# Optimization experiments

Hardware: AMD Instinct MI355X
Metric: run time of the kernel (lower is better)

Reference implementation:

```python
import jax, jax.numpy as jnp
import numpy as np

GENES = 20000   # input gene nodes (depth 0)
LEVEL = 10000   # nodes per subsequent depth level
STEPS = 7       # depth propagation steps
DEG = 16        # in-degree per dst node
N = GENES + STEPS * LEVEL          # 90000 total nodes
EPS = LEVEL * DEG                  # 160000 edges per step
E = STEPS * EPS                    # 1120000 total edges
B = 256
C = 2


def setup_inputs() -> dict:
    key = jax.random.key(0)
    k0, k1, k2 = jax.random.split(key, 3)
    X = jax.random.normal(k0, (B, GENES), jnp.float32)
    gene_map = jnp.arange(GENES, dtype=jnp.int32)

    rng = np.random.default_rng(0)
    src_list, dstu_list = [], []
    for k in range(STEPS):
        lo = 0 if k == 0 else GENES + (k - 1) * LEVEL
        hi = GENES if k == 0 else lo + LEVEL
        src_list.append(rng.integers(lo, hi, size=EPS))
        dstu_list.append(np.arange(GENES + k * LEVEL, GENES + (k + 1) * LEVEL))
    src = jnp.asarray(np.stack(src_list), dtype=jnp.int32)          # [STEPS, EPS]
    dst_unique = jnp.asarray(np.stack(dstu_list), dtype=jnp.int32)  # [STEPS, LEVEL]
    dst_pos = jnp.tile(jnp.repeat(jnp.arange(LEVEL, dtype=jnp.int32), DEG)[None, :], (STEPS, 1))
    eid = jnp.arange(E, dtype=jnp.int32).reshape(STEPS, EPS)
    root_ids = dst_unique[-1]

    edge_weight = jax.random.normal(k1, (E,), jnp.float32) * 0.01
    node_bias = jnp.zeros((N,), jnp.float32)
    head_W = jax.random.normal(k2, (LEVEL, C), jnp.float32) * (1.0 / np.sqrt(LEVEL))
    head_b = jnp.zeros((C,), jnp.float32)

    return dict(X=X, edge_weight=edge_weight, node_bias=node_bias,
                head_W=head_W, head_b=head_b, gene_map=gene_map,
                src=src, dst_pos=dst_pos, dst_unique=dst_unique,
                eid=eid, root_ids=root_ids)


def reference(X, edge_weight, node_bias, head_W, head_b,
              gene_map, src, dst_pos, dst_unique, eid, root_ids):
    # dropout is identity (eval mode / p=0)
    b = X.shape[0]
    h = jnp.zeros((b, N), X.dtype).at[:, gene_map].set(X)
    for k in range(src.shape[0]):  # fixed small number of depth steps
        w = edge_weight[eid[k]]                                   # [EPS]
        msg = h[:, src[k]] * w[None, :]                           # gather + scale [B, EPS]
        agg = jnp.zeros((b, dst_unique.shape[1]), h.dtype).at[:, dst_pos[k]].add(msg)
        h_dst = jnp.tanh(agg + node_bias[dst_unique[k]][None, :])  # [B, LEVEL]
        h = h.at[:, dst_unique[k]].set(h_dst)
    roots = h[:, root_ids]                                        # [B, LEVEL]
    return roots @ head_W + head_b
```

## Files before the change

kernel.cpp:

```cpp
#include <hip/hip_runtime.h>
#include <math.h>

#define GENES 20000
#define LEVEL 10000
#define STEPS 7
#define DEG   16
#define EPSZ  (LEVEL * DEG)
#define CCOLS 32
#define NCHUNK 8
#define SBLK  157
#define DBLK  313
#define NGT   625
#define MSTRIDE 18

typedef unsigned short bf8 __attribute__((ext_vector_type(8)));

__device__ inline float bf2f(unsigned short u) {
    union { unsigned u; float f; } c; c.u = ((unsigned)u) << 16; return c.f;
}
__device__ inline unsigned short f2bf(float x) {
    union { float f; unsigned u; } c; c.f = x;
    return (unsigned short)((c.u + 0x7fffu + ((c.u >> 16) & 1u)) >> 16);
}

__global__ __launch_bounds__(256) void transpose_k(const float* __restrict__ X,
                                                   const int*   __restrict__ gene_map,
                                                   unsigned short* __restrict__ XT) {
    __shared__ float tile[32][33];
    const int chunk = blockIdx.x;
    const int l4  = threadIdx.x & 7;
    const int r8  = threadIdx.x >> 3;
    const int lo  = threadIdx.x & 31;
    const int gr8 = threadIdx.x >> 5;
    unsigned short* XTp = XT + (size_t)chunk * GENES * CCOLS;
    for (int i = 0; i < 4; ++i) {
        const int gt = blockIdx.y * 4 + i;
        if (gt >= NGT) break;
        const int g0 = gt * 32;
        if (i) __syncthreads();
        const float4 xv = *reinterpret_cast<const float4*>(
            X + (size_t)(chunk * CCOLS + r8) * GENES + g0 + l4 * 4);
        tile[r8][l4 * 4 + 0] = xv.x;
        tile[r8][l4 * 4 + 1] = xv.y;
        tile[r8][l4 * 4 + 2] = xv.z;
        tile[r8][l4 * 4 + 3] = xv.w;
        __syncthreads();
#pragma unroll
        for (int jj = 0; jj < 4; ++jj) {
            const int gr   = gr8 + jj * 8;
            const int node = gene_map[g0 + gr];
            XTp[(size_t)node * CCOLS + lo] = f2bf(tile[lo][gr]);
        }
    }
}

__global__ __launch_bounds__(256) void step_k(const unsigned short* __restrict__ hprev,
                                              unsigned short*       __restrict__ hcur,
                                              const int*   __restrict__ src_k,
                                              const float* __restrict__ w_k,
                                              const float* __restrict__ node_bias,
                                              const int*   __restrict__ dstu_k,
                                              int src_base, int prev_rows) {
    const int bid   = blockIdx.x;
    const int chunk = bid & 7;
    const int cb    = bid >> 3;
    const int tid   = threadIdx.x;

    __shared__ int   s_src[32 * MSTRIDE];
    __shared__ float s_w  [32 * MSTRIDE];

    if (tid < 128) {
        const int m4 = cb * 128 + tid;
        if (m4 < EPSZ / 4) {
            const int4 sv = reinterpret_cast<const int4*>(src_k)[m4];
            const int j = tid >> 2, i = (tid & 3) * 4;
            *reinterpret_cast<int4*>(&s_src[j * MSTRIDE + i]) = sv;
        }
    } else {
        const int t  = tid - 128;
        const int m4 = cb * 128 + t;
        if (m4 < EPSZ / 4) {
            const float4 wv = reinterpret_cast<const float4*>(w_k)[m4];
            const int j = t >> 2, i = (t & 3) * 4;
            *reinterpret_cast<float4*>(&s_w[j * MSTRIDE + i]) = wv;
        }
    }
    __syncthreads();

    const int wave = tid >> 6, lane = tid & 63;
    const int c2 = lane & 3;
    const int eh = (lane >> 2) & 1;
    const int q  = lane >> 3;
    const int j  = wave * 8 + q;
    const int dest = cb * 32 + j;
    const int c8 = c2 * 8;

    if (dest < LEVEL) {
        const unsigned short* prev = hprev + (size_t)chunk * prev_rows * CCOLS;
        unsigned short*       curp = hcur + (size_t)chunk * LEVEL * CCOLS;

        const int mb = j * MSTRIDE + eh * 8;
        const int4   sA = *reinterpret_cast<const int4*>  (&s_src[mb]);
        const int4   sB = *reinterpret_cast<const int4*>  (&s_src[mb + 4]);
        const float4 wA = *reinterpret_cast<const float4*>(&s_w  [mb]);
        const float4 wB = *reinterpret_cast<const float4*>(&s_w  [mb + 4]);

#define GL(sv) (*reinterpret_cast<const bf8*>(prev + (size_t)((sv) - src_base) * CCOLS + c8))
        const bf8 v0 = GL(sA.x);
        const bf8 v1 = GL(sA.y);
        const bf8 v2 = GL(sA.z);
        const bf8 v3 = GL(sA.w);
        const bf8 v4 = GL(sB.x);
        const bf8 v5 = GL(sB.y);
        const bf8 v6 = GL(sB.z);
        const bf8 v7 = GL(sB.w);
#undef GL

        float a0 = 0.f, a1 = 0.f, a2 = 0.f, a3 = 0.f, a4 = 0.f, a5 = 0.f, a6 = 0.f, a7 = 0.f;
#define FMA8(v, wv) { a0 = fmaf(bf2f((v)[0]), (wv), a0); a1 = fmaf(bf2f((v)[1]), (wv), a1);  \
                      a2 = fmaf(bf2f((v)[2]), (wv), a2); a3 = fmaf(bf2f((v)[3]), (wv), a3);  \
                      a4 = fmaf(bf2f((v)[4]), (wv), a4); a5 = fmaf(bf2f((v)[5]), (wv), a5);  \
                      a6 = fmaf(bf2f((v)[6]), (wv), a6); a7 = fmaf(bf2f((v)[7]), (wv), a7); }
        FMA8(v0, wA.x) FMA8(v1, wA.y) FMA8(v2, wA.z) FMA8(v3, wA.w)
        FMA8(v4, wB.x) FMA8(v5, wB.y) FMA8(v6, wB.z) FMA8(v7, wB.w)
#undef FMA8

        a0 += __shfl_xor(a0, 4); a1 += __shfl_xor(a1, 4);
        a2 += __shfl_xor(a2, 4); a3 += __shfl_xor(a3, 4);
        a4 += __shfl_xor(a4, 4); a5 += __shfl_xor(a5, 4);
        a6 += __shfl_xor(a6, 4); a7 += __shfl_xor(a7, 4);

        if (eh == 0) {
            const float bz = node_bias[dstu_k[dest]];
            bf8 o;
            o[0] = f2bf(tanhf(a0 + bz));
            o[1] = f2bf(tanhf(a1 + bz));
            o[2] = f2bf(tanhf(a2 + bz));
            o[3] = f2bf(tanhf(a3 + bz));
            o[4] = f2bf(tanhf(a4 + bz));
            o[5] = f2bf(tanhf(a5 + bz));
            o[6] = f2bf(tanhf(a6 + bz));
            o[7] = f2bf(tanhf(a7 + bz));
            *reinterpret_cast<bf8*>(curp + (size_t)dest * CCOLS + c8) = o;
        }
    }
}

__global__ __launch_bounds__(256) void step7_head_k(const unsigned short* __restrict__ hprev,
                                                    const int*   __restrict__ src_k,
                                                    const float* __restrict__ w_k,
                                                    const float* __restrict__ node_bias,
                                                    const int*   __restrict__ dstu_k,
                                                    const float* __restrict__ head_W,
                                                    float*       __restrict__ part,
                                                    int src_base) {
    const int bid   = blockIdx.x;
    const int chunk = bid & 7;
    const int cb    = bid >> 3;
    const int tid   = threadIdx.x;

    __shared__ int   s_src[64 * MSTRIDE];
    __shared__ float s_w  [64 * MSTRIDE];
    __shared__ float o_tile[64][33];
    __shared__ float s_W2[64][2];
    __shared__ float red[8][64];

    {
        const int m4 = cb * 256 + tid;
        if (m4 < EPSZ / 4) {
            const int4   sv = reinterpret_cast<const int4*>(src_k)[m4];
            const float4 wv = reinterpret_cast<const float4*>(w_k)[m4];
            const int j = tid >> 2, i = (tid & 3) * 4;
            *reinterpret_cast<int4*>  (&s_src[j * MSTRIDE + i]) = sv;
            *reinterpret_cast<float4*>(&s_w  [j * MSTRIDE + i]) = wv;
        }
    }
    if (tid < 32) {
        const int f4 = cb * 32 + tid;
        float4 wv = make_float4(0.f, 0.f, 0.f, 0.f);
        if (f4 < (LEVEL * 2) / 4) wv = reinterpret_cast<const float4*>(head_W)[f4];
        s_W2[tid * 2 + 0][0] = wv.x; s_W2[tid * 2 + 0][1] = wv.y;
        s_W2[tid * 2 + 1][0] = wv.z; s_W2[tid * 2 + 1][1] = wv.w;
    }
    __syncthreads();

    const int wave = tid >> 6, lane = tid & 63;
    const int q    = lane >> 2;
    const int c8   = (lane & 3) * 8;
    const int j    = wave * 16 + q;
    const int dest = cb * 64 + j;

    const unsigned short* prev = hprev + (size_t)chunk * LEVEL * CCOLS;

    float o0 = 0.f, o1 = 0.f, o2 = 0.f, o3 = 0.f, o4 = 0.f, o5 = 0.f, o6 = 0.f, o7 = 0.f;
    if (dest < LEVEL) {
        const int4   s0 = *reinterpret_cast<const int4*>  (&s_src[j * MSTRIDE + 0]);
        const int4   s1 = *reinterpret_cast<const int4*>  (&s_src[j * MSTRIDE + 4]);
        const int4   s2 = *reinterpret_cast<const int4*>  (&s_src[j * MSTRIDE + 8]);
        const int4   s3 = *reinterpret_cast<const int4*>  (&s_src[j * MSTRIDE + 12]);
        const float4 w0 = *reinterpret_cast<const float4*>(&s_w  [j * MSTRIDE + 0]);
        const float4 w1 = *reinterpret_cast<const float4*>(&s_w  [j * MSTRIDE + 4]);
        const float4 w2 = *reinterpret_cast<const float4*>(&s_w  [j * MSTRIDE + 8]);
        const float4 w3 = *reinterpret_cast<const float4*>(&s_w  [j * MSTRIDE + 12]);

        float a0 = 0.f, a1 = 0.f, a2 = 0.f, a3 = 0.f, a4 = 0.f, a5 = 0.f, a6 = 0.f, a7 = 0.f;
#define ACC(sv, wv) { const int idx = (sv) - src_base;                                      \
    const bf8 v = *reinterpret_cast<const bf8*>(prev + (size_t)idx * CCOLS + c8);           \
    a0 = fmaf(bf2f(v[0]), (wv), a0); a1 = fmaf(bf2f(v[1]), (wv), a1);                       \
    a2 = fmaf(bf2f(v[2]), (wv), a2); a3 = fmaf(bf2f(v[3]), (wv), a3);                       \
    a4 = fmaf(bf2f(v[4]), (wv), a4); a5 = fmaf(bf2f(v[5]), (wv), a5);                       \
    a6 = fmaf(bf2f(v[6]), (wv), a6); a7 = fmaf(bf2f(v[7]), (wv), a7); }
        ACC(s0.x, w0.x) ACC(s0.y, w0.y) ACC(s0.z, w0.z) ACC(s0.w, w0.w)
        ACC(s1.x, w1.x) ACC(s1.y, w1.y) ACC(s1.z, w1.z) ACC(s1.w, w1.w)
        ACC(s2.x, w2.x) ACC(s2.y, w2.y) ACC(s2.z, w2.z) ACC(s2.w, w2.w)
        ACC(s3.x, w3.x) ACC(s3.y, w3.y) ACC(s3.z, w3.z) ACC(s3.w, w3.w)
#undef ACC
        const float bz = node_bias[dstu_k[dest]];
        o0 = tanhf(a0 + bz); o1 = tanhf(a1 + bz); o2 = tanhf(a2 + bz); o3 = tanhf(a3 + bz);
        o4 = tanhf(a4 + bz); o5 = tanhf(a5 + bz); o6 = tanhf(a6 + bz); o7 = tanhf(a7 + bz);
    }
    o_tile[j][c8 + 0] = o0; o_tile[j][c8 + 1] = o1;
    o_tile[j][c8 + 2] = o2; o_tile[j][c8 + 3] = o3;
    o_tile[j][c8 + 4] = o4; o_tile[j][c8 + 5] = o5;
    o_tile[j][c8 + 6] = o6; o_tile[j][c8 + 7] = o7;
    __syncthreads();

    {
        const int col = tid & 31, slot = tid >> 5;
        float a0 = 0.f, a1 = 0.f;
#pragma unroll
        for (int e = 0; e < 8; ++e) {
            const int jj = slot * 8 + e;
            const float v = o_tile[jj][col];
            a0 = fmaf(v, s_W2[jj][0], a0);
            a1 = fmaf(v, s_W2[jj][1], a1);
        }
        red[slot][col * 2 + 0] = a0;
        red[slot][col * 2 + 1] = a1;
    }
    __syncthreads();
    if (tid < 64) {
        float s = 0.f;
#pragma unroll
        for (int p = 0; p < 8; ++p) s += red[p][tid];
        part[((size_t)chunk * SBLK + cb) * 64 + tid] = s;
    }
}

__global__ __launch_bounds__(64) void head_final_k(const float* __restrict__ part,
                                                   const float* __restrict__ head_b,
                                                   float*       __restrict__ out) {
    const int chunk = blockIdx.x;
    const int t     = threadIdx.x;
    float acc = head_b[t & 1];
    for (int q = 0; q < SBLK; ++q)
        acc += part[((size_t)chunk * SBLK + q) * 64 + t];
    out[chunk * 64 + t] = acc;
}

extern "C" void kernel_launch(void* const* d_in, const int* in_sizes, int n_in,
                              void* d_out, int out_size, void* d_ws, size_t ws_size,
                              hipStream_t stream) {
    const float* X           = (const float*)d_in[0];
    const float* edge_weight = (const float*)d_in[1];
    const float* node_bias   = (const float*)d_in[2];
    const float* head_W      = (const float*)d_in[3];
    const float* head_b      = (const float*)d_in[4];
    const int*   gene_map    = (const int*)  d_in[5];
    const int*   src         = (const int*)  d_in[6];
    const int*   dst_unique  = (const int*)  d_in[8];
    float* out = (float*)d_out;

    char* ws = (char*)d_ws;
    unsigned short* XT   = (unsigned short*)(ws);
    unsigned short* lvlA = (unsigned short*)(ws + 10240000);
    unsigned short* lvlB = (unsigned short*)(ws + 15360000);
    float*          part = (float*)         (ws + 20480000);

    transpose_k<<<dim3(NCHUNK, 157), 256, 0, stream>>>(X, gene_map, XT);

    unsigned short* bufs[2] = {lvlA, lvlB};
    for (int k = 0; k < STEPS - 1; ++k) {
        const unsigned short* hprev = (k == 0) ? XT : bufs[(k - 1) & 1];
        const int prevrows = (k == 0) ? GENES : LEVEL;
        const int srcbase  = (k == 0) ? 0 : GENES + (k - 1) * LEVEL;
        step_k<<<DBLK * NCHUNK, 256, 0, stream>>>(hprev, bufs[k & 1],
                                                  src + (size_t)k * EPSZ,
                                                  edge_weight + (size_t)k * EPSZ,
                                                  node_bias,
                                                  dst_unique + (size_t)k * LEVEL,
                                                  srcbase, prevrows);
    }

    {
        const int k = STEPS - 1;
        const unsigned short* hprev = bufs[(k - 1) & 1];
        const int srcbase = GENES + (k - 1) * LEVEL;
        step7_head_k<<<SBLK * NCHUNK, 256, 0, stream>>>(hprev,
                                                        src + (size_t)k * EPSZ,
                                                        edge_weight + (size_t)k * EPSZ,
                                                        node_bias,
                                                        dst_unique + (size_t)k * LEVEL,
                                                        head_W, part, srcbase);
        head_final_k<<<NCHUNK, 64, 0, stream>>>(part, head_b, out);
    }
    (void)in_sizes; (void)n_in; (void)out_size; (void)ws_size;
}
```

Before: 91.31 us.

## Stage level slices in LDS and gather from shared memory for steps 2-7

```diff
diff --git a/kernel.cpp b/kernel.cpp
--- a/kernel.cpp
+++ b/kernel.cpp
@@ -8,10 +8,13 @@
 #define EPSZ  (LEVEL * DEG)
 #define CCOLS 32
 #define NCHUNK 8
-#define SBLK  157
 #define DBLK  313
 #define NGT   625
 #define MSTRIDE 18
+#define SCOLS 8
+#define NCC   32
+#define GPB   8
+#define DPB   1250
 
 typedef unsigned short bf8 __attribute__((ext_vector_type(8)));
 
@@ -21,6 +24,46 @@
 __device__ inline unsigned short f2bf(float x) {
     union { float f; unsigned u; } c; c.f = x;
     return (unsigned short)((c.u + 0x7fffu + ((c.u >> 16) & 1u)) >> 16);
+}
+
+__global__ __launch_bounds__(256) void prep_k(const int*   __restrict__ src,
+                                              const float* __restrict__ ew,
+                                              unsigned short* __restrict__ srcT,
+                                              float*          __restrict__ wT) {
+    const int kk = blockIdx.y;
+    const int b  = blockIdx.x;
+    const int t  = threadIdx.x;
+    const int base = GENES + kk * LEVEL;
+    __shared__ unsigned short s_i[256][DEG + 1];
+    __shared__ float          s_w[256][DEG + 1];
+    const int*   sk = src + (size_t)(kk + 1) * EPSZ + (size_t)b * 256 * DEG;
+    const float* wk = ew  + (size_t)(kk + 1) * EPSZ + (size_t)b * 256 * DEG;
+    const int lim4 = (EPSZ - b * 256 * DEG) / 4;
+#pragma unroll
+    for (int i = 0; i < 4; ++i) {
+        const int m4 = i * 256 + t;
+        if (m4 >= lim4) continue;
+        const int4   sv = reinterpret_cast<const int4*>(sk)[m4];
+        const float4 wv = reinterpret_cast<const float4*>(wk)[m4];
+        const int dl = m4 >> 2, e0 = (m4 & 3) * 4;
+        s_i[dl][e0 + 0] = (unsigned short)(sv.x - base);
+        s_i[dl][e0 + 1] = (unsigned short)(sv.y - base);
+        s_i[dl][e0 + 2] = (unsigned short)(sv.z - base);
+        s_i[dl][e0 + 3] = (unsigned short)(sv.w - base);
+        s_w[dl][e0 + 0] = wv.x;
+        s_w[dl][e0 + 1] = wv.y;
+        s_w[dl][e0 + 2] = wv.z;
+        s_w[dl][e0 + 3] = wv.w;
+    }
+    __syncthreads();
+    const int dg = b * 256;
+    if (dg + t < LEVEL) {
+#pragma unroll
+        for (int e = 0; e < DEG; ++e) {
+            srcT[((size_t)kk * DEG + e) * LEVEL + dg + t] = s_i[t][e];
+            wT  [((size_t)kk * DEG + e) * LEVEL + dg + t] = s_w[t][e];
+        }
+    }
 }
 
 __global__ __launch_bounds__(256) void transpose_k(const float* __restrict__ X,
@@ -54,13 +97,12 @@
     }
 }
 
-__global__ __launch_bounds__(256) void step_k(const unsigned short* __restrict__ hprev,
-                                              unsigned short*       __restrict__ hcur,
-                                              const int*   __restrict__ src_k,
-                                              const float* __restrict__ w_k,
-                                              const float* __restrict__ node_bias,
-                                              const int*   __restrict__ dstu_k,
-                                              int src_base, int prev_rows) {
+__global__ __launch_bounds__(256) void step1_k(const unsigned short* __restrict__ hprev,
+                                               unsigned short*       __restrict__ hcur,
+                                               const int*   __restrict__ src_k,
+                                               const float* __restrict__ w_k,
+                                               const float* __restrict__ node_bias,
+                                               const int*   __restrict__ dstu_k) {
     const int bid   = blockIdx.x;
     const int chunk = bid & 7;
     const int cb    = bid >> 3;
@@ -96,8 +138,7 @@
     const int c8 = c2 * 8;
 
     if (dest < LEVEL) {
-        const unsigned short* prev = hprev + (size_t)chunk * prev_rows * CCOLS;
-        unsigned short*       curp = hcur + (size_t)chunk * LEVEL * CCOLS;
+        const unsigned short* prev = hprev + (size_t)chunk * GENES * CCOLS;
 
         const int mb = j * MSTRIDE + eh * 8;
         const int4   sA = *reinterpret_cast<const int4*>  (&s_src[mb]);
@@ -105,7 +146,7 @@
         const float4 wA = *reinterpret_cast<const float4*>(&s_w  [mb]);
         const float4 wB = *reinterpret_cast<const float4*>(&s_w  [mb + 4]);
 
-#define GL(sv) (*reinterpret_cast<const bf8*>(prev + (size_t)((sv) - src_base) * CCOLS + c8))
+#define GL(sv) (*reinterpret_cast<const bf8*>(prev + (size_t)(sv) * CCOLS + c8))
         const bf8 v0 = GL(sA.x);
         const bf8 v1 = GL(sA.y);
         const bf8 v2 = GL(sA.z);
@@ -115,7 +156,6 @@
         const bf8 v6 = GL(sB.z);
         const bf8 v7 = GL(sB.w);
 #undef GL
-
         float a0 = 0.f, a1 = 0.f, a2 = 0.f, a3 = 0.f, a4 = 0.f, a5 = 0.f, a6 = 0.f, a7 = 0.f;
 #define FMA8(v, wv) { a0 = fmaf(bf2f((v)[0]), (wv), a0); a1 = fmaf(bf2f((v)[1]), (wv), a1);  \
                       a2 = fmaf(bf2f((v)[2]), (wv), a2); a3 = fmaf(bf2f((v)[3]), (wv), a3);  \
@@ -124,7 +164,6 @@
         FMA8(v0, wA.x) FMA8(v1, wA.y) FMA8(v2, wA.z) FMA8(v3, wA.w)
         FMA8(v4, wB.x) FMA8(v5, wB.y) FMA8(v6, wB.z) FMA8(v7, wB.w)
 #undef FMA8
-
         a0 += __shfl_xor(a0, 4); a1 += __shfl_xor(a1, 4);
         a2 += __shfl_xor(a2, 4); a3 += __shfl_xor(a3, 4);
         a4 += __shfl_xor(a4, 4); a5 += __shfl_xor(a5, 4);
@@ -141,121 +180,156 @@
             o[5] = f2bf(tanhf(a5 + bz));
             o[6] = f2bf(tanhf(a6 + bz));
             o[7] = f2bf(tanhf(a7 + bz));
-            *reinterpret_cast<bf8*>(curp + (size_t)dest * CCOLS + c8) = o;
-        }
-    }
-}
-
-__global__ __launch_bounds__(256) void step7_head_k(const unsigned short* __restrict__ hprev,
-                                                    const int*   __restrict__ src_k,
-                                                    const float* __restrict__ w_k,
-                                                    const float* __restrict__ node_bias,
-                                                    const int*   __restrict__ dstu_k,
-                                                    const float* __restrict__ head_W,
-                                                    float*       __restrict__ part,
-                                                    int src_base) {
-    const int bid   = blockIdx.x;
-    const int chunk = bid & 7;
-    const int cb    = bid >> 3;
-    const int tid   = threadIdx.x;
-
-    __shared__ int   s_src[64 * MSTRIDE];
-    __shared__ float s_w  [64 * MSTRIDE];
-    __shared__ float o_tile[64][33];
-    __shared__ float s_W2[64][2];
-    __shared__ float red[8][64];
-
-    {
-        const int m4 = cb * 256 + tid;
-        if (m4 < EPSZ / 4) {
-            const int4   sv = reinterpret_cast<const int4*>(src_k)[m4];
-            const float4 wv = reinterpret_cast<const float4*>(w_k)[m4];
-            const int j = tid >> 2, i = (tid & 3) * 4;
-            *reinterpret_cast<int4*>  (&s_src[j * MSTRIDE + i]) = sv;
-            *reinterpret_cast<float4*>(&s_w  [j * MSTRIDE + i]) = wv;
-        }
-    }
-    if (tid < 32) {
-        const int f4 = cb * 32 + tid;
-        float4 wv = make_float4(0.f, 0.f, 0.f, 0.f);
-        if (f4 < (LEVEL * 2) / 4) wv = reinterpret_cast<const float4*>(head_W)[f4];
-        s_W2[tid * 2 + 0][0] = wv.x; s_W2[tid * 2 + 0][1] = wv.y;
-        s_W2[tid * 2 + 1][0] = wv.z; s_W2[tid * 2 + 1][1] = wv.w;
-    }
-    __syncthreads();
-
-    const int wave = tid >> 6, lane = tid & 63;
-    const int q    = lane >> 2;
-    const int c8   = (lane & 3) * 8;
-    const int j    = wave * 16 + q;
-    const int dest = cb * 64 + j;
-
-    const unsigned short* prev = hprev + (size_t)chunk * LEVEL * CCOLS;
-
-    float o0 = 0.f, o1 = 0.f, o2 = 0.f, o3 = 0.f, o4 = 0.f, o5 = 0.f, o6 = 0.f, o7 = 0.f;
-    if (dest < LEVEL) {
-        const int4   s0 = *reinterpret_cast<const int4*>  (&s_src[j * MSTRIDE + 0]);
-        const int4   s1 = *reinterpret_cast<const int4*>  (&s_src[j * MSTRIDE + 4]);
-        const int4   s2 = *reinterpret_cast<const int4*>  (&s_src[j * MSTRIDE + 8]);
-        const int4   s3 = *reinterpret_cast<const int4*>  (&s_src[j * MSTRIDE + 12]);
-        const float4 w0 = *reinterpret_cast<const float4*>(&s_w  [j * MSTRIDE + 0]);
-        const float4 w1 = *reinterpret_cast<const float4*>(&s_w  [j * MSTRIDE + 4]);
-        const float4 w2 = *reinterpret_cast<const float4*>(&s_w  [j * MSTRIDE + 8]);
-        const float4 w3 = *reinterpret_cast<const float4*>(&s_w  [j * MSTRIDE + 12]);
-
+            *reinterpret_cast<bf8*>(hcur + ((size_t)(chunk * 4 + c2) * LEVEL + dest) * SCOLS) = o;
+        }
+    }
+}
+
+__global__ __launch_bounds__(256, 1) void sstep_k(
+        const unsigned short* __restrict__ hprev,
+        unsigned short*       __restrict__ hcur,
+        const unsigned short* __restrict__ srcT,
+        const float*          __restrict__ wT,
+        const float* __restrict__ node_bias,
+        const int*   __restrict__ dstu_k) {
+    __shared__ unsigned short slice[LEVEL * SCOLS];
+    const int bid = blockIdx.x;
+    const int c   = (bid & 7) * 4 + ((bid >> 3) & 3);
+    const int g   = bid >> 5;
+    const int tid = threadIdx.x;
+
+    const unsigned short* pc = hprev + (size_t)c * LEVEL * SCOLS;
+#pragma unroll 4
+    for (int i = 0; i < 40; ++i) {
+        const int row = i * 256 + tid;
+        if (row < LEVEL)
+            *reinterpret_cast<bf8*>(&slice[row * SCOLS]) =
+                *reinterpret_cast<const bf8*>(pc + (size_t)row * SCOLS);
+    }
+    __syncthreads();
+
+    unsigned short* oc = hcur + (size_t)c * LEVEL * SCOLS;
+    const int dbeg = g * DPB, dend = dbeg + DPB;
+    for (int d = dbeg + tid; d < dend; d += 256) {
+        int   idx[DEG];
+        float w[DEG];
+#pragma unroll
+        for (int e = 0; e < DEG; ++e) idx[e] = srcT[e * LEVEL + d];
+#pragma unroll
+        for (int e = 0; e < DEG; ++e) w[e] = wT[e * LEVEL + d];
         float a0 = 0.f, a1 = 0.f, a2 = 0.f, a3 = 0.f, a4 = 0.f, a5 = 0.f, a6 = 0.f, a7 = 0.f;
-#define ACC(sv, wv) { const int idx = (sv) - src_base;                                      \
-    const bf8 v = *reinterpret_cast<const bf8*>(prev + (size_t)idx * CCOLS + c8);           \
-    a0 = fmaf(bf2f(v[0]), (wv), a0); a1 = fmaf(bf2f(v[1]), (wv), a1);                       \
-    a2 = fmaf(bf2f(v[2]), (wv), a2); a3 = fmaf(bf2f(v[3]), (wv), a3);                       \
-    a4 = fmaf(bf2f(v[4]), (wv), a4); a5 = fmaf(bf2f(v[5]), (wv), a5);                       \
-    a6 = fmaf(bf2f(v[6]), (wv), a6); a7 = fmaf(bf2f(v[7]), (wv), a7); }
-        ACC(s0.x, w0.x) ACC(s0.y, w0.y) ACC(s0.z, w0.z) ACC(s0.w, w0.w)
-        ACC(s1.x, w1.x) ACC(s1.y, w1.y) ACC(s1.z, w1.z) ACC(s1.w, w1.w)
-        ACC(s2.x, w2.x) ACC(s2.y, w2.y) ACC(s2.z, w2.z) ACC(s2.w, w2.w)
-        ACC(s3.x, w3.x) ACC(s3.y, w3.y) ACC(s3.z, w3.z) ACC(s3.w, w3.w)
-#undef ACC
-        const float bz = node_bias[dstu_k[dest]];
-        o0 = tanhf(a0 + bz); o1 = tanhf(a1 + bz); o2 = tanhf(a2 + bz); o3 = tanhf(a3 + bz);
-        o4 = tanhf(a4 + bz); o5 = tanhf(a5 + bz); o6 = tanhf(a6 + bz); o7 = tanhf(a7 + bz);
-    }
-    o_tile[j][c8 + 0] = o0; o_tile[j][c8 + 1] = o1;
-    o_tile[j][c8 + 2] = o2; o_tile[j][c8 + 3] = o3;
-    o_tile[j][c8 + 4] = o4; o_tile[j][c8 + 5] = o5;
-    o_tile[j][c8 + 6] = o6; o_tile[j][c8 + 7] = o7;
-    __syncthreads();
-
-    {
-        const int col = tid & 31, slot = tid >> 5;
-        float a0 = 0.f, a1 = 0.f;
-#pragma unroll
-        for (int e = 0; e < 8; ++e) {
-            const int jj = slot * 8 + e;
-            const float v = o_tile[jj][col];
-            a0 = fmaf(v, s_W2[jj][0], a0);
-            a1 = fmaf(v, s_W2[jj][1], a1);
-        }
-        red[slot][col * 2 + 0] = a0;
-        red[slot][col * 2 + 1] = a1;
-    }
-    __syncthreads();
-    if (tid < 64) {
-        float s = 0.f;
-#pragma unroll
-        for (int p = 0; p < 8; ++p) s += red[p][tid];
-        part[((size_t)chunk * SBLK + cb) * 64 + tid] = s;
-    }
-}
-
-__global__ __launch_bounds__(64) void head_final_k(const float* __restrict__ part,
-                                                   const float* __restrict__ head_b,
-                                                   float*       __restrict__ out) {
-    const int chunk = blockIdx.x;
-    const int t     = threadIdx.x;
-    float acc = head_b[t & 1];
-    for (int q = 0; q < SBLK; ++q)
-        acc += part[((size_t)chunk * SBLK + q) * 64 + t];
-    out[chunk * 64 + t] = acc;
+#pragma unroll
+        for (int e = 0; e < DEG; ++e) {
+            const bf8 v = *reinterpret_cast<const bf8*>(&slice[idx[e] * SCOLS]);
+            a0 = fmaf(bf2f(v[0]), w[e], a0); a1 = fmaf(bf2f(v[1]), w[e], a1);
+            a2 = fmaf(bf2f(v[2]), w[e], a2); a3 = fmaf(bf2f(v[3]), w[e], a3);
+            a4 = fmaf(bf2f(v[4]), w[e], a4); a5 = fmaf(bf2f(v[5]), w[e], a5);
+            a6 = fmaf(bf2f(v[6]), w[e], a6); a7 = fmaf(bf2f(v[7]), w[e], a7);
+        }
+        const float bz = node_bias[dstu_k[d]];
+        bf8 o;
+        o[0] = f2bf(tanhf(a0 + bz));
+        o[1] = f2bf(tanhf(a1 + bz));
+        o[2] = f2bf(tanhf(a2 + bz));
+        o[3] = f2bf(tanhf(a3 + bz));
+        o[4] = f2bf(tanhf(a4 + bz));
+        o[5] = f2bf(tanhf(a5 + bz));
+        o[6] = f2bf(tanhf(a6 + bz));
+        o[7] = f2bf(tanhf(a7 + bz));
+        *reinterpret_cast<bf8*>(oc + (size_t)d * SCOLS) = o;
+    }
+}
+
+__global__ __launch_bounds__(256, 1) void sstep7_k(
+        const unsigned short* __restrict__ hprev,
+        const unsigned short* __restrict__ srcT,
+        const float*          __restrict__ wT,
+        const float* __restrict__ node_bias,
+        const int*   __restrict__ dstu_k,
+        const float* __restrict__ head_W,
+        float*       __restrict__ part) {
+    __shared__ unsigned short slice[LEVEL * SCOLS];
+    __shared__ float scratch[4][16];
+    const int bid = blockIdx.x;
+    const int c   = (bid & 7) * 4 + ((bid >> 3) & 3);
+    const int g   = bid >> 5;
+    const int tid = threadIdx.x;
+
+    const unsigned short* pc = hprev + (size_t)c * LEVEL * SCOLS;
+#pragma unroll 4
+    for (int i = 0; i < 40; ++i) {
+        const int row = i * 256 + tid;
+        if (row < LEVEL)
+            *reinterpret_cast<bf8*>(&slice[row * SCOLS]) =
+                *reinterpret_cast<const bf8*>(pc + (size_t)row * SCOLS);
+    }
+    __syncthreads();
+
+    float h[16];
+#pragma unroll
+    for (int j = 0; j < 16; ++j) h[j] = 0.f;
+
+    const int dbeg = g * DPB, dend = dbeg + DPB;
+    for (int d = dbeg + tid; d < dend; d += 256) {
+        int   idx[DEG];
+        float w[DEG];
+#pragma unroll
+        for (int e = 0; e < DEG; ++e) idx[e] = srcT[e * LEVEL + d];
+#pragma unroll
+        for (int e = 0; e < DEG; ++e) w[e] = wT[e * LEVEL + d];
+        float a0 = 0.f, a1 = 0.f, a2 = 0.f, a3 = 0.f, a4 = 0.f, a5 = 0.f, a6 = 0.f, a7 = 0.f;
+#pragma unroll
+        for (int e = 0; e < DEG; ++e) {
+            const bf8 v = *reinterpret_cast<const bf8*>(&slice[idx[e] * SCOLS]);
+            a0 = fmaf(bf2f(v[0]), w[e], a0); a1 = fmaf(bf2f(v[1]), w[e], a1);
+            a2 = fmaf(bf2f(v[2]), w[e], a2); a3 = fmaf(bf2f(v[3]), w[e], a3);
+            a4 = fmaf(bf2f(v[4]), w[e], a4); a5 = fmaf(bf2f(v[5]), w[e], a5);
+            a6 = fmaf(bf2f(v[6]), w[e], a6); a7 = fmaf(bf2f(v[7]), w[e], a7);
+        }
+        const float bz = node_bias[dstu_k[d]];
+        const float o0 = tanhf(a0 + bz), o1 = tanhf(a1 + bz);
+        const float o2 = tanhf(a2 + bz), o3 = tanhf(a3 + bz);
+        const float o4 = tanhf(a4 + bz), o5 = tanhf(a5 + bz);
+        const float o6 = tanhf(a6 + bz), o7 = tanhf(a7 + bz);
+        const float2 wv = *reinterpret_cast<const float2*>(head_W + (size_t)d * 2);
+        h[0]  = fmaf(o0, wv.x, h[0]);  h[1]  = fmaf(o0, wv.y, h[1]);
+        h[2]  = fmaf(o1, wv.x, h[2]);  h[3]  = fmaf(o1, wv.y, h[3]);
+        h[4]  = fmaf(o2, wv.x, h[4]);  h[5]  = fmaf(o2, wv.y, h[5]);
+        h[6]  = fmaf(o3, wv.x, h[6]);  h[7]  = fmaf(o3, wv.y, h[7]);
+        h[8]  = fmaf(o4, wv.x, h[8]);  h[9]  = fmaf(o4, wv.y, h[9]);
+        h[10] = fmaf(o5, wv.x, h[10]); h[11] = fmaf(o5, wv.y, h[11]);
+        h[12] = fmaf(o6, wv.x, h[12]); h[13] = fmaf(o6, wv.y, h[13]);
+        h[14] = fmaf(o7, wv.x, h[14]); h[15] = fmaf(o7, wv.y, h[15]);
+    }
+
+    const int wv_ = tid >> 6, lane = tid & 63;
+#pragma unroll
+    for (int m = 1; m < 64; m <<= 1) {
+#pragma unroll
+        for (int j = 0; j < 16; ++j) h[j] += __shfl_xor(h[j], m);
+    }
+    if (lane == 0) {
+#pragma unroll
+        for (int j = 0; j < 16; ++j) scratch[wv_][j] = h[j];
+    }
+    __syncthreads();
+    if (tid < 16) {
+        const float s = scratch[0][tid] + scratch[1][tid] + scratch[2][tid] + scratch[3][tid];
+        part[((size_t)c * GPB + g) * 16 + tid] = s;
+    }
+}
+
+__global__ __launch_bounds__(512) void head_final_k(const float* __restrict__ part,
+                                                    const float* __restrict__ head_b,
+                                                    float*       __restrict__ out) {
+    const int tid = threadIdx.x;
+    const int cc = tid >> 4, v = tid & 15;
+    float acc = head_b[v & 1];
+#pragma unroll
+    for (int g = 0; g < GPB; ++g)
+        acc += part[((size_t)cc * GPB + g) * 16 + v];
+    const int b = (cc >> 2) * 32 + (cc & 3) * 8 + (v >> 1);
+    out[b * 2 + (v & 1)] = acc;
 }
 
 extern "C" void kernel_launch(void* const* d_in, const int* in_sizes, int n_in,
@@ -272,37 +346,35 @@
     float* out = (float*)d_out;
 
     char* ws = (char*)d_ws;
-    unsigned short* XT   = (unsigned short*)(ws);
-    unsigned short* lvlA = (unsigned short*)(ws + 10240000);
-    unsigned short* lvlB = (unsigned short*)(ws + 15360000);
-    float*          part = (float*)         (ws + 20480000);
+    unsigned short* XT    = (unsigned short*)(ws);
+    unsigned short* lvlA  = (unsigned short*)(ws + 10240000);
+    unsigned short* lvlB  = (unsigned short*)(ws + 15360000);
+    unsigned short* srcT  = (unsigned short*)(ws + 20480000);
+    float*          wT    = (float*)         (ws + 22400000);
+    float*          part  = (float*)         (ws + 26240000);
+
+    prep_k<<<dim3(40, 6), 256, 0, stream>>>(src, edge_weight, srcT, wT);
 
     transpose_k<<<dim3(NCHUNK, 157), 256, 0, stream>>>(X, gene_map, XT);
 
+    step1_k<<<DBLK * NCHUNK, 256, 0, stream>>>(XT, lvlA, src, edge_weight,
+                                               node_bias, dst_unique);
+
     unsigned short* bufs[2] = {lvlA, lvlB};
-    for (int k = 0; k < STEPS - 1; ++k) {
-        const unsigned short* hprev = (k == 0) ? XT : bufs[(k - 1) & 1];
-        const int prevrows = (k == 0) ? GENES : LEVEL;
-        const int srcbase  = (k == 0) ? 0 : GENES + (k - 1) * LEVEL;
-        step_k<<<DBLK * NCHUNK, 256, 0, stream>>>(hprev, bufs[k & 1],
-                                                  src + (size_t)k * EPSZ,
-                                                  edge_weight + (size_t)k * EPSZ,
-                                                  node_bias,
-                                                  dst_unique + (size_t)k * LEVEL,
-                                                  srcbase, prevrows);
-    }
-
-    {
-        const int k = STEPS - 1;
-        const unsigned short* hprev = bufs[(k - 1) & 1];
-        const int srcbase = GENES + (k - 1) * LEVEL;
-        step7_head_k<<<SBLK * NCHUNK, 256, 0, stream>>>(hprev,
-                                                        src + (size_t)k * EPSZ,
-                                                        edge_weight + (size_t)k * EPSZ,
-                                                        node_bias,
-                                                        dst_unique + (size_t)k * LEVEL,
-                                                        head_W, part, srcbase);
-        head_final_k<<<NCHUNK, 64, 0, stream>>>(part, head_b, out);
-    }
+    for (int k = 1; k <= 5; ++k) {
+        sstep_k<<<NCC * GPB, 256, 0, stream>>>(bufs[(k - 1) & 1], bufs[k & 1],
+                                               srcT + (size_t)(k - 1) * DEG * LEVEL,
+                                               wT   + (size_t)(k - 1) * DEG * LEVEL,
+                                               node_bias,
+                                               dst_unique + (size_t)k * LEVEL);
+    }
+
+    sstep7_k<<<NCC * GPB, 256, 0, stream>>>(bufs[5 & 1],
+                                            srcT + (size_t)5 * DEG * LEVEL,
+                                            wT   + (size_t)5 * DEG * LEVEL,
+                                            node_bias,
+                                            dst_unique + (size_t)6 * LEVEL,
+                                            head_W, part);
+    head_final_k<<<1, 512, 0, stream>>>(part, head_b, out);
     (void)in_sizes; (void)n_in; (void)out_size; (void)ws_size;
 }
```

New measurement: 148.6 us. 62.8% more time.

## Widen batch chunks to 64 columns and fuse head reduction via shuffles

Applied to the files above, without the earlier changes.

```diff
diff --git a/kernel.cpp b/kernel.cpp
--- a/kernel.cpp
+++ b/kernel.cpp
@@ -6,10 +6,9 @@
 #define STEPS 7
 #define DEG   16
 #define EPSZ  (LEVEL * DEG)
-#define CCOLS 32
-#define NCHUNK 8
-#define SBLK  157
-#define DBLK  313
+#define CCOLS 64
+#define NCHUNK 4
+#define SBLK7 313
 #define NGT   625
 #define MSTRIDE 18
 
@@ -27,19 +26,21 @@
                                                    const int*   __restrict__ gene_map,
                                                    unsigned short* __restrict__ XT) {
     __shared__ float tile[32][33];
-    const int chunk = blockIdx.x;
-    const int l4  = threadIdx.x & 7;
-    const int r8  = threadIdx.x >> 3;
-    const int lo  = threadIdx.x & 31;
-    const int gr8 = threadIdx.x >> 5;
-    unsigned short* XTp = XT + (size_t)chunk * GENES * CCOLS;
+    const int bt   = blockIdx.x;
+    const int l4   = threadIdx.x & 7;
+    const int r8   = threadIdx.x >> 3;
+    const int lo   = threadIdx.x & 31;
+    const int gr8  = threadIdx.x >> 5;
+    const int chunk = bt >> 1;
+    const int coff  = (bt & 1) * 32;
+    unsigned short* XTp = XT + (size_t)chunk * GENES * CCOLS + coff;
     for (int i = 0; i < 4; ++i) {
         const int gt = blockIdx.y * 4 + i;
         if (gt >= NGT) break;
         const int g0 = gt * 32;
         if (i) __syncthreads();
         const float4 xv = *reinterpret_cast<const float4*>(
-            X + (size_t)(chunk * CCOLS + r8) * GENES + g0 + l4 * 4);
+            X + (size_t)(bt * 32 + r8) * GENES + g0 + l4 * 4);
         tile[r8][l4 * 4 + 0] = xv.x;
         tile[r8][l4 * 4 + 1] = xv.y;
         tile[r8][l4 * 4 + 2] = xv.z;
@@ -62,12 +63,96 @@
                                               const int*   __restrict__ dstu_k,
                                               int src_base, int prev_rows) {
     const int bid   = blockIdx.x;
-    const int chunk = bid & 7;
-    const int cb    = bid >> 3;
+    const int chunk = bid & 3;
+    const int cb    = bid >> 2;
+    const int tid   = threadIdx.x;
+
+    __shared__ int   s_src[16 * MSTRIDE];
+    __shared__ float s_w  [16 * MSTRIDE];
+
+    if (tid < 64) {
+        const int4 sv = reinterpret_cast<const int4*>(src_k)[cb * 64 + tid];
+        const int j = tid >> 2, i = (tid & 3) * 4;
+        *reinterpret_cast<int4*>(&s_src[j * MSTRIDE + i]) = sv;
+    } else if (tid < 128) {
+        const int t = tid - 64;
+        const float4 wv = reinterpret_cast<const float4*>(w_k)[cb * 64 + t];
+        const int j = t >> 2, i = (t & 3) * 4;
+        *reinterpret_cast<float4*>(&s_w[j * MSTRIDE + i]) = wv;
+    }
+    __syncthreads();
+
+    const int wave = tid >> 6, lane = tid & 63;
+    const int c16 = (lane & 7) * 8;
+    const int eh  = (lane >> 3) & 1;
+    const int q   = lane >> 4;
+    const int j   = wave * 4 + q;
+    const int dest = cb * 16 + j;
+
+    const unsigned short* prev = hprev + (size_t)chunk * prev_rows * CCOLS;
+    unsigned short*       curp = hcur + (size_t)chunk * LEVEL * CCOLS;
+
+    const int mb = j * MSTRIDE + eh * 8;
+    const int4   sA = *reinterpret_cast<const int4*>  (&s_src[mb]);
+    const int4   sB = *reinterpret_cast<const int4*>  (&s_src[mb + 4]);
+    const float4 wA = *reinterpret_cast<const float4*>(&s_w  [mb]);
+    const float4 wB = *reinterpret_cast<const float4*>(&s_w  [mb + 4]);
+
+#define GL(sv) (*reinterpret_cast<const bf8*>(prev + (size_t)((sv) - src_base) * CCOLS + c16))
+    const bf8 v0 = GL(sA.x);
+    const bf8 v1 = GL(sA.y);
+    const bf8 v2 = GL(sA.z);
+    const bf8 v3 = GL(sA.w);
+    const bf8 v4 = GL(sB.x);
+    const bf8 v5 = GL(sB.y);
+    const bf8 v6 = GL(sB.z);
+    const bf8 v7 = GL(sB.w);
+#undef GL
+    float a0 = 0.f, a1 = 0.f, a2 = 0.f, a3 = 0.f, a4 = 0.f, a5 = 0.f, a6 = 0.f, a7 = 0.f;
+#define FMA8(v, wv) { a0 = fmaf(bf2f((v)[0]), (wv), a0); a1 = fmaf(bf2f((v)[1]), (wv), a1);  \
+                      a2 = fmaf(bf2f((v)[2]), (wv), a2); a3 = fmaf(bf2f((v)[3]), (wv), a3);  \
+                      a4 = fmaf(bf2f((v)[4]), (wv), a4); a5 = fmaf(bf2f((v)[5]), (wv), a5);  \
+                      a6 = fmaf(bf2f((v)[6]), (wv), a6); a7 = fmaf(bf2f((v)[7]), (wv), a7); }
+    FMA8(v0, wA.x) FMA8(v1, wA.y) FMA8(v2, wA.z) FMA8(v3, wA.w)
+    FMA8(v4, wB.x) FMA8(v5, wB.y) FMA8(v6, wB.z) FMA8(v7, wB.w)
+#undef FMA8
+
+    a0 += __shfl_xor(a0, 8); a1 += __shfl_xor(a1, 8);
+    a2 += __shfl_xor(a2, 8); a3 += __shfl_xor(a3, 8);
+    a4 += __shfl_xor(a4, 8); a5 += __shfl_xor(a5, 8);
+    a6 += __shfl_xor(a6, 8); a7 += __shfl_xor(a7, 8);
+
+    if (eh == 0) {
+        const float bz = node_bias[dstu_k[dest]];
+        bf8 o;
+        o[0] = f2bf(tanhf(a0 + bz));
+        o[1] = f2bf(tanhf(a1 + bz));
+        o[2] = f2bf(tanhf(a2 + bz));
+        o[3] = f2bf(tanhf(a3 + bz));
+        o[4] = f2bf(tanhf(a4 + bz));
+        o[5] = f2bf(tanhf(a5 + bz));
+        o[6] = f2bf(tanhf(a6 + bz));
+        o[7] = f2bf(tanhf(a7 + bz));
+        *reinterpret_cast<bf8*>(curp + (size_t)dest * CCOLS + c16) = o;
+    }
+}
+
+__global__ __launch_bounds__(256) void step7_head_k(const unsigned short* __restrict__ hprev,
+                                                    const int*   __restrict__ src_k,
+                                                    const float* __restrict__ w_k,
+                                                    const float* __restrict__ node_bias,
+                                                    const int*   __restrict__ dstu_k,
+                                                    const float* __restrict__ head_W,
+                                                    float*       __restrict__ part,
+                                                    int src_base) {
+    const int bid   = blockIdx.x;
+    const int chunk = bid & 3;
+    const int cb    = bid >> 2;
     const int tid   = threadIdx.x;
 
     __shared__ int   s_src[32 * MSTRIDE];
     __shared__ float s_w  [32 * MSTRIDE];
+    __shared__ float red[4][8][16];
 
     if (tid < 128) {
         const int m4 = cb * 128 + tid;
@@ -88,111 +173,17 @@
     __syncthreads();
 
     const int wave = tid >> 6, lane = tid & 63;
-    const int c2 = lane & 3;
-    const int eh = (lane >> 2) & 1;
-    const int q  = lane >> 3;
-    const int j  = wave * 8 + q;
+    const int c16 = (lane & 7) * 8;
+    const int q   = lane >> 3;
+    const int j   = wave * 8 + q;
     const int dest = cb * 32 + j;
-    const int c8 = c2 * 8;
-
-    if (dest < LEVEL) {
-        const unsigned short* prev = hprev + (size_t)chunk * prev_rows * CCOLS;
-        unsigned short*       curp = hcur + (size_t)chunk * LEVEL * CCOLS;
-
-        const int mb = j * MSTRIDE + eh * 8;
-        const int4   sA = *reinterpret_cast<const int4*>  (&s_src[mb]);
-        const int4   sB = *reinterpret_cast<const int4*>  (&s_src[mb + 4]);
-        const float4 wA = *reinterpret_cast<const float4*>(&s_w  [mb]);
-        const float4 wB = *reinterpret_cast<const float4*>(&s_w  [mb + 4]);
-
-#define GL(sv) (*reinterpret_cast<const bf8*>(prev + (size_t)((sv) - src_base) * CCOLS + c8))
-        const bf8 v0 = GL(sA.x);
-        const bf8 v1 = GL(sA.y);
-        const bf8 v2 = GL(sA.z);
-        const bf8 v3 = GL(sA.w);
-        const bf8 v4 = GL(sB.x);
-        const bf8 v5 = GL(sB.y);
-        const bf8 v6 = GL(sB.z);
-        const bf8 v7 = GL(sB.w);
-#undef GL
-
-        float a0 = 0.f, a1 = 0.f, a2 = 0.f, a3 = 0.f, a4 = 0.f, a5 = 0.f, a6 = 0.f, a7 = 0.f;
-#define FMA8(v, wv) { a0 = fmaf(bf2f((v)[0]), (wv), a0); a1 = fmaf(bf2f((v)[1]), (wv), a1);  \
-                      a2 = fmaf(bf2f((v)[2]), (wv), a2); a3 = fmaf(bf2f((v)[3]), (wv), a3);  \
-                      a4 = fmaf(bf2f((v)[4]), (wv), a4); a5 = fmaf(bf2f((v)[5]), (wv), a5);  \
-                      a6 = fmaf(bf2f((v)[6]), (wv), a6); a7 = fmaf(bf2f((v)[7]), (wv), a7); }
-        FMA8(v0, wA.x) FMA8(v1, wA.y) FMA8(v2, wA.z) FMA8(v3, wA.w)
-        FMA8(v4, wB.x) FMA8(v5, wB.y) FMA8(v6, wB.z) FMA8(v7, wB.w)
-#undef FMA8
-
-        a0 += __shfl_xor(a0, 4); a1 += __shfl_xor(a1, 4);
-        a2 += __shfl_xor(a2, 4); a3 += __shfl_xor(a3, 4);
-        a4 += __shfl_xor(a4, 4); a5 += __shfl_xor(a5, 4);
-        a6 += __shfl_xor(a6, 4); a7 += __shfl_xor(a7, 4);
-
-        if (eh == 0) {
-            const float bz = node_bias[dstu_k[dest]];
-            bf8 o;
-            o[0] = f2bf(tanhf(a0 + bz));
-            o[1] = f2bf(tanhf(a1 + bz));
-            o[2] = f2bf(tanhf(a2 + bz));
-            o[3] = f2bf(tanhf(a3 + bz));
-            o[4] = f2bf(tanhf(a4 + bz));
-            o[5] = f2bf(tanhf(a5 + bz));
-            o[6] = f2bf(tanhf(a6 + bz));
-            o[7] = f2bf(tanhf(a7 + bz));
-            *reinterpret_cast<bf8*>(curp + (size_t)dest * CCOLS + c8) = o;
-        }
-    }
-}
-
-__global__ __launch_bounds__(256) void step7_head_k(const unsigned short* __restrict__ hprev,
-                                                    const int*   __restrict__ src_k,
-                                                    const float* __restrict__ w_k,
-                                                    const float* __restrict__ node_bias,
-                                                    const int*   __restrict__ dstu_k,
-                                                    const float* __restrict__ head_W,
-                                                    float*       __restrict__ part,
-                                                    int src_base) {
-    const int bid   = blockIdx.x;
-    const int chunk = bid & 7;
-    const int cb    = bid >> 3;
-    const int tid   = threadIdx.x;
-
-    __shared__ int   s_src[64 * MSTRIDE];
-    __shared__ float s_w  [64 * MSTRIDE];
-    __shared__ float o_tile[64][33];
-    __shared__ float s_W2[64][2];
-    __shared__ float red[8][64];
-
-    {
-        const int m4 = cb * 256 + tid;
-        if (m4 < EPSZ / 4) {
-            const int4   sv = reinterpret_cast<const int4*>(src_k)[m4];
-            const float4 wv = reinterpret_cast<const float4*>(w_k)[m4];
-            const int j = tid >> 2, i = (tid & 3) * 4;
-            *reinterpret_cast<int4*>  (&s_src[j * MSTRIDE + i]) = sv;
-            *reinterpret_cast<float4*>(&s_w  [j * MSTRIDE + i]) = wv;
-        }
-    }
-    if (tid < 32) {
-        const int f4 = cb * 32 + tid;
-        float4 wv = make_float4(0.f, 0.f, 0.f, 0.f);
-        if (f4 < (LEVEL * 2) / 4) wv = reinterpret_cast<const float4*>(head_W)[f4];
-        s_W2[tid * 2 + 0][0] = wv.x; s_W2[tid * 2 + 0][1] = wv.y;
-        s_W2[tid * 2 + 1][0] = wv.z; s_W2[tid * 2 + 1][1] = wv.w;
-    }
-    __syncthreads();
-
-    const int wave = tid >> 6, lane = tid & 63;
-    const int q    = lane >> 2;
-    const int c8   = (lane & 3) * 8;
-    const int j    = wave * 16 + q;
-    const int dest = cb * 64 + j;
 
     const unsigned short* prev = hprev + (size_t)chunk * LEVEL * CCOLS;
 
-    float o0 = 0.f, o1 = 0.f, o2 = 0.f, o3 = 0.f, o4 = 0.f, o5 = 0.f, o6 = 0.f, o7 = 0.f;
+    float h[16];
+#pragma unroll
+    for (int v = 0; v < 16; ++v) h[v] = 0.f;
+
     if (dest < LEVEL) {
         const int4   s0 = *reinterpret_cast<const int4*>  (&s_src[j * MSTRIDE + 0]);
         const int4   s1 = *reinterpret_cast<const int4*>  (&s_src[j * MSTRIDE + 4]);
@@ -205,7 +196,7 @@
 
         float a0 = 0.f, a1 = 0.f, a2 = 0.f, a3 = 0.f, a4 = 0.f, a5 = 0.f, a6 = 0.f, a7 = 0.f;
 #define ACC(sv, wv) { const int idx = (sv) - src_base;                                      \
-    const bf8 v = *reinterpret_cast<const bf8*>(prev + (size_t)idx * CCOLS + c8);           \
+    const bf8 v = *reinterpret_cast<const bf8*>(prev + (size_t)idx * CCOLS + c16);          \
     a0 = fmaf(bf2f(v[0]), (wv), a0); a1 = fmaf(bf2f(v[1]), (wv), a1);                       \
     a2 = fmaf(bf2f(v[2]), (wv), a2); a3 = fmaf(bf2f(v[3]), (wv), a3);                       \
     a4 = fmaf(bf2f(v[4]), (wv), a4); a5 = fmaf(bf2f(v[5]), (wv), a5);                       \
@@ -216,46 +207,49 @@
         ACC(s3.x, w3.x) ACC(s3.y, w3.y) ACC(s3.z, w3.z) ACC(s3.w, w3.w)
 #undef ACC
         const float bz = node_bias[dstu_k[dest]];
-        o0 = tanhf(a0 + bz); o1 = tanhf(a1 + bz); o2 = tanhf(a2 + bz); o3 = tanhf(a3 + bz);
-        o4 = tanhf(a4 + bz); o5 = tanhf(a5 + bz); o6 = tanhf(a6 + bz); o7 = tanhf(a7 + bz);
-    }
-    o_tile[j][c8 + 0] = o0; o_tile[j][c8 + 1] = o1;
-    o_tile[j][c8 + 2] = o2; o_tile[j][c8 + 3] = o3;
-    o_tile[j][c8 + 4] = o4; o_tile[j][c8 + 5] = o5;
-    o_tile[j][c8 + 6] = o6; o_tile[j][c8 + 7] = o7;
+        const float o0 = tanhf(a0 + bz), o1 = tanhf(a1 + bz);
+        const float o2 = tanhf(a2 + bz), o3 = tanhf(a3 + bz);
+        const float o4 = tanhf(a4 + bz), o5 = tanhf(a5 + bz);
+        const float o6 = tanhf(a6 + bz), o7 = tanhf(a7 + bz);
+        const float2 wv = *reinterpret_cast<const float2*>(head_W + (size_t)dest * 2);
+        h[0]  = o0 * wv.x; h[1]  = o0 * wv.y;
+        h[2]  = o1 * wv.x; h[3]  = o1 * wv.y;
+        h[4]  = o2 * wv.x; h[5]  = o2 * wv.y;
+        h[6]  = o3 * wv.x; h[7]  = o3 * wv.y;
+        h[8]  = o4 * wv.x; h[9]  = o4 * wv.y;
+        h[10] = o5 * wv.x; h[11] = o5 * wv.y;
+        h[12] = o6 * wv.x; h[13] = o6 * wv.y;
+        h[14] = o7 * wv.x; h[15] = o7 * wv.y;
+    }
+
+#pragma unroll
+    for (int m = 8; m < 64; m <<= 1) {
+#pragma unroll
+        for (int v = 0; v < 16; ++v) h[v] += __shfl_xor(h[v], m);
+    }
+    if (lane < 8) {
+#pragma unroll
+        for (int v = 0; v < 16; ++v) red[wave][lane][v] = h[v];
+    }
     __syncthreads();
-
-    {
-        const int col = tid & 31, slot = tid >> 5;
-        float a0 = 0.f, a1 = 0.f;
-#pragma unroll
-        for (int e = 0; e < 8; ++e) {
-            const int jj = slot * 8 + e;
-            const float v = o_tile[jj][col];
-            a0 = fmaf(v, s_W2[jj][0], a0);
-            a1 = fmaf(v, s_W2[jj][1], a1);
-        }
-        red[slot][col * 2 + 0] = a0;
-        red[slot][col * 2 + 1] = a1;
-    }
-    __syncthreads();
-    if (tid < 64) {
-        float s = 0.f;
-#pragma unroll
-        for (int p = 0; p < 8; ++p) s += red[p][tid];
-        part[((size_t)chunk * SBLK + cb) * 64 + tid] = s;
-    }
-}
-
-__global__ __launch_bounds__(64) void head_final_k(const float* __restrict__ part,
-                                                   const float* __restrict__ head_b,
-                                                   float*       __restrict__ out) {
-    const int chunk = blockIdx.x;
-    const int t     = threadIdx.x;
-    float acc = head_b[t & 1];
-    for (int q = 0; q < SBLK; ++q)
-        acc += part[((size_t)chunk * SBLK + q) * 64 + t];
-    out[chunk * 64 + t] = acc;
+    if (tid < 128) {
+        const int cg = tid >> 4, v = tid & 15;
+        const float s = red[0][cg][v] + red[1][cg][v] + red[2][cg][v] + red[3][cg][v];
+        part[(size_t)bid * 128 + tid] = s;
+    }
+}
+
+__global__ __launch_bounds__(512) void head_final_k(const float* __restrict__ part,
+                                                    const float* __restrict__ head_b,
+                                                    float*       __restrict__ out) {
+    const int tid = threadIdx.x;
+    const int chunk = tid >> 7, r = tid & 127;
+    float acc = head_b[r & 1];
+    for (int cb = 0; cb < SBLK7; ++cb)
+        acc += part[(size_t)(cb * NCHUNK + chunk) * 128 + r];
+    const int cg = r >> 4, v = r & 15;
+    const int b = chunk * 64 + cg * 8 + (v >> 1);
+    out[b * 2 + (v & 1)] = acc;
 }
 
 extern "C" void kernel_launch(void* const* d_in, const int* in_sizes, int n_in,
@@ -277,32 +271,32 @@
     unsigned short* lvlB = (unsigned short*)(ws + 15360000);
     float*          part = (float*)         (ws + 20480000);
 
-    transpose_k<<<dim3(NCHUNK, 157), 256, 0, stream>>>(X, gene_map, XT);
+    transpose_k<<<dim3(8, 157), 256, 0, stream>>>(X, gene_map, XT);
 
     unsigned short* bufs[2] = {lvlA, lvlB};
     for (int k = 0; k < STEPS - 1; ++k) {
         const unsigned short* hprev = (k == 0) ? XT : bufs[(k - 1) & 1];
         const int prevrows = (k == 0) ? GENES : LEVEL;
         const int srcbase  = (k == 0) ? 0 : GENES + (k - 1) * LEVEL;
-        step_k<<<DBLK * NCHUNK, 256, 0, stream>>>(hprev, bufs[k & 1],
-                                                  src + (size_t)k * EPSZ,
-                                                  edge_weight + (size_t)k * EPSZ,
-                                                  node_bias,
-                                                  dst_unique + (size_t)k * LEVEL,
-                                                  srcbase, prevrows);
+        step_k<<<625 * NCHUNK, 256, 0, stream>>>(hprev, bufs[k & 1],
+                                                 src + (size_t)k * EPSZ,
+                                                 edge_weight + (size_t)k * EPSZ,
+                                                 node_bias,
+                                                 dst_unique + (size_t)k * LEVEL,
+                                                 srcbase, prevrows);
     }
 
     {
         const int k = STEPS - 1;
         const unsigned short* hprev = bufs[(k - 1) & 1];
         const int srcbase = GENES + (k - 1) * LEVEL;
-        step7_head_k<<<SBLK * NCHUNK, 256, 0, stream>>>(hprev,
-                                                        src + (size_t)k * EPSZ,
-                                                        edge_weight + (size_t)k * EPSZ,
-                                                        node_bias,
-                                                        dst_unique + (size_t)k * LEVEL,
-                                                        head_W, part, srcbase);
-        head_final_k<<<NCHUNK, 64, 0, stream>>>(part, head_b, out);
+        step7_head_k<<<SBLK7 * NCHUNK, 256, 0, stream>>>(hprev,
+                                                         src + (size_t)k * EPSZ,
+                                                         edge_weight + (size_t)k * EPSZ,
+                                                         node_bias,
+                                                         dst_unique + (size_t)k * LEVEL,
+                                                         head_W, part, srcbase);
+        head_final_k<<<1, 512, 0, stream>>>(part, head_b, out);
     }
     (void)in_sizes; (void)n_in; (void)out_size; (void)ws_size;
 }
```

Result: slower. 99.46 us (+8.9%).
